# Kernel tuning notes

Hardware: AMD Instinct MI355X
Metric: run time of the kernel (lower is better)

## Reference

```python
import jax, jax.numpy as jnp
import numpy as np

EPS = 1e-6
NUM_HEADS = 16


def layer_norm(x, a, b):
    # Faithful to the custom LayerNorm: unbiased std (ddof=1), eps added to sigma.
    mu = jnp.mean(x, axis=-1, keepdims=True)
    sigma = jnp.std(x, axis=-1, keepdims=True, ddof=1) + EPS
    return (x - mu) / sigma * a + b


def entmax15(x):
    # Exact 1.5-entmax along the last axis (Peters et al. 2019, sort-based).
    S = x.shape[-1]
    x = x / 2.0
    x = x - jnp.max(x, axis=-1, keepdims=True)  # shift-invariant stabilization
    xs = jnp.flip(jnp.sort(x, axis=-1), axis=-1)  # descending
    k = jnp.arange(1, S + 1, dtype=x.dtype)
    mean = jnp.cumsum(xs, axis=-1) / k
    meansq = jnp.cumsum(xs * xs, axis=-1) / k
    ss = k * (meansq - mean * mean)
    delta = (1.0 - ss) / k
    tau = mean - jnp.sqrt(jnp.clip(delta, 0.0))
    support_size = jnp.sum((tau <= xs).astype(jnp.int32), axis=-1, keepdims=True)
    tau_star = jnp.take_along_axis(tau, support_size - 1, axis=-1)
    return jnp.clip(x - tau_star, 0.0) ** 2


def linear(x, w, b):
    return jnp.einsum('bsd,od->bso', x, w) + b


def setup_inputs() -> dict:
    key = jax.random.key(0)
    B, S, D, DFF = 1, 2048, 1024, 4096
    ks = jax.random.split(key, 12)
    p = lambda k, shape: jax.random.normal(k, shape, dtype=jnp.float32) * 0.02
    return {
        'inputs': jax.random.normal(ks[0], (B, S, D), dtype=jnp.float32),
        'mask': jax.random.randint(ks[1], (B, S), 0, 2, dtype=jnp.int32),
        'wq': p(ks[2], (D, D)), 'bq': jnp.zeros((D,), jnp.float32),
        'wk': p(ks[3], (D, D)), 'bk': jnp.zeros((D,), jnp.float32),
        'wv': p(ks[4], (D, D)), 'bv': jnp.zeros((D,), jnp.float32),
        'wo': p(ks[5], (D, D)), 'bo': jnp.zeros((D,), jnp.float32),
        'ln1_a': jnp.ones((D,), jnp.float32), 'ln1_b': jnp.zeros((D,), jnp.float32),
        'w1': p(ks[6], (DFF, D)), 'b1': jnp.zeros((DFF,), jnp.float32),
        'w2': p(ks[7], (D, DFF)), 'b2': jnp.zeros((D,), jnp.float32),
        'ln2_a': jnp.ones((D,), jnp.float32), 'ln2_b': jnp.zeros((D,), jnp.float32),
    }


def reference(inputs, mask, wq, bq, wk, bk, wv, bv, wo, bo, ln1_a, ln1_b,
              w1, b1, w2, b2, ln2_a, ln2_b):
    B, S, D = inputs.shape
    H = NUM_HEADS
    hd = D // H

    # --- Sublayer 1: pre-norm -> SparseMHA -> residual (dropout=0 -> identity) ---
    x1 = layer_norm(inputs, ln1_a, ln1_b)
    split = lambda t: t.reshape(B, S, H, hd).transpose(0, 2, 1, 3)  # [B,H,S,hd]
    q = split(linear(x1, wq, bq))
    k = split(linear(x1, wk, bk))
    v = split(linear(x1, wv, bv))

    scores = jnp.einsum('bhqd,bhkd->bhqk', q, k) / jnp.sqrt(jnp.asarray(hd, jnp.float32))
    # torch: mask.unsqueeze(0) -> (1,B,S); with B==1 it broadcasts as a key mask (1,1,1,S)
    mask4 = mask[None, None]  # (1,1,B,S), B==1
    scores = jnp.where(mask4 == 0, jnp.float32(-1e9), scores)

    p_attn = entmax15(scores).astype(jnp.float32)
    attended = jnp.einsum('bhqk,bhkd->bhqd', p_attn, v)
    attended = attended.transpose(0, 2, 1, 3).reshape(B, S, D)
    y = inputs + linear(attended, wo, bo)

    # --- Sublayer 2: pre-norm -> FFN -> residual ---
    x2 = layer_norm(y, ln2_a, ln2_b)
    ffn = linear(jax.nn.relu(linear(x2, w1, b1)), w2, b2)
    return y + ffn
```

## Files before the change

kernel.cpp:

```cpp
#include <hip/hip_runtime.h>
#include <hip/hip_bf16.h>

#define S   2048
#define D   1024
#define DFF 4096
#define NH  16
#define HD  64

typedef unsigned short u16;
typedef unsigned int   u32;
typedef __attribute__((ext_vector_type(8))) short      short8;
typedef __attribute__((ext_vector_type(4))) float      floatx4;
typedef __attribute__((ext_vector_type(2))) _Float16   half2v;
typedef __attribute__((ext_vector_type(4))) _Float16   half4v;
typedef __attribute__((ext_vector_type(8))) _Float16   half8v;

__device__ __forceinline__ float bu2f(u16 u) {
    union { u32 i; float f; } x; x.i = ((u32)u) << 16; return x.f;
}
__device__ __forceinline__ u16 f2bu(float f) {
    __hip_bfloat16 h = __float2bfloat16(f);
    return *(u16*)&h;
}
__device__ __forceinline__ u16 f2h(float f) {
    _Float16 h = (_Float16)f; return *(u16*)&h;
}
__device__ __forceinline__ float ldf(const float* p) { return *p; }
__device__ __forceinline__ float ldf(const u16* p)   { return bu2f(*p); }

__device__ __forceinline__ half2v pkrtz(float a, float b) {
    auto v = __builtin_amdgcn_cvt_pkrtz(a, b);
    union { decltype(v) i; half2v o; } u; u.i = v; return u.o;
}

__device__ __forceinline__ floatx4 mfma_f16(half8v a, half8v b, floatx4 c) {
    return __builtin_amdgcn_mfma_f32_16x16x32_f16(a, b, c, 0, 0, 0);
}
__device__ __forceinline__ float fdot2f(half2v a, half2v b, float c) {
#if __has_builtin(__builtin_amdgcn_fdot2)
    return __builtin_amdgcn_fdot2(a, b, c, false);
#else
    return c + (float)a[0] * (float)b[0] + (float)a[1] * (float)b[1];
#endif
}

template <int K>
__device__ __forceinline__ float ror16f(float v) {
    int s = __builtin_bit_cast(int, v);
    int r = __builtin_amdgcn_update_dpp(s, s, 0x120 | K, 0xF, 0xF, false);
    return __builtin_bit_cast(float, r);
}
__device__ __forceinline__ float rowsum16(float v) {
    v += ror16f<1>(v);
    v += ror16f<2>(v);
    v += ror16f<4>(v);
    v += ror16f<8>(v);
    return v;
}
__device__ __forceinline__ float rowmax16(float v) {
    v = fmaxf(v, ror16f<1>(v));
    v = fmaxf(v, ror16f<2>(v));
    v = fmaxf(v, ror16f<4>(v));
    v = fmaxf(v, ror16f<8>(v));
    return v;
}

__device__ __forceinline__ void async16(const void* g, void* l) {
    __builtin_amdgcn_global_load_lds(
        (const __attribute__((address_space(1))) u32*)g,
        (__attribute__((address_space(3))) u32*)l, 16, 0, 0);
}

__global__ __launch_bounds__(256)
void cvt_kernel(const float* __restrict__ in, u16* __restrict__ out, int n4)
{
    int i = blockIdx.x * 256 + threadIdx.x;
    if (i < n4) {
        float4 v = ((const float4*)in)[i];
        ushort4 s;
        s.x = f2bu(v.x); s.y = f2bu(v.y); s.z = f2bu(v.z); s.w = f2bu(v.w);
        ((ushort4*)out)[i] = s;
    }
}

__global__ __launch_bounds__(256)
void scan_mask_kernel(const int* __restrict__ mask, int* __restrict__ newpos,
                      int* __restrict__ nkbuf)
{
    __shared__ int ps[256];
    const int t = threadIdx.x;
    int loc[8];
    int s = 0;
#pragma unroll
    for (int j = 0; j < 8; j++) {
        loc[j] = s;
        s += (mask[t * 8 + j] != 0);
    }
    ps[t] = s;
    __syncthreads();
    for (int off = 1; off < 256; off <<= 1) {
        int v = (t >= off) ? ps[t - off] : 0;
        __syncthreads();
        ps[t] += v;
        __syncthreads();
    }
    const int total = ps[255];
    const int base = t ? ps[t - 1] : 0;
#pragma unroll
    for (int j = 0; j < 8; j++) {
        const int gi = t * 8 + j;
        const int up = base + loc[j];
        newpos[gi] = mask[gi] ? up : (total + gi - up);
    }
    if (t == 0) nkbuf[0] = total;
}

template <typename T>
__global__ __launch_bounds__(256, 4)
void ln_kernel(const T* __restrict__ in, const float* __restrict__ ga,
               const float* __restrict__ gb, u16* __restrict__ out)
{
    const int row = blockIdx.x;
    const int t = threadIdx.x;
    const T* x = in + (size_t)row * D;
    float v[4];
    float s = 0.f, ss = 0.f;
#pragma unroll
    for (int j = 0; j < 4; j++) {
        float val = ldf(x + t + 256 * j);
        v[j] = val; s += val; ss = fmaf(val, val, ss);
    }
#pragma unroll
    for (int off = 32; off >= 1; off >>= 1) {
        s  += __shfl_down(s,  off, 64);
        ss += __shfl_down(ss, off, 64);
    }
    __shared__ float red[10];
    const int wave = t >> 6, lane = t & 63;
    if (lane == 0) { red[wave] = s; red[4 + wave] = ss; }
    __syncthreads();
    if (t == 0) {
        float S1 = red[0] + red[1] + red[2] + red[3];
        float S2 = red[4] + red[5] + red[6] + red[7];
        float mu = S1 / (float)D;
        float var = (S2 - (float)D * mu * mu) / (float)(D - 1);
        float sig = sqrtf(fmaxf(var, 0.f)) + 1e-6f;
        red[8] = mu; red[9] = 1.f / sig;
    }
    __syncthreads();
    const float mu = red[8], rs = red[9];
#pragma unroll
    for (int j = 0; j < 4; j++) {
        int c = t + 256 * j;
        out[(size_t)row * D + c] = f2bu((v[j] - mu) * rs * ga[c] + gb[c]);
    }
}

#define GEMM_CORE(A_, B_, K_)                                                   \
    __shared__ u16 As[128 * 32];                                                \
    __shared__ u16 Bs[128 * 32];                                                \
    const int t = threadIdx.x;                                                  \
    const int w = t >> 6, l = t & 63;                                           \
    const int m0 = blockIdx.y * 128, n0 = blockIdx.x * 128;                     \
    const int qk = l >> 4, col = l & 15;                                        \
    const int wm = (w & 1) * 64, wn = (w >> 1) * 64;                            \
    const int sr  = l >> 2;                                                     \
    const int sq  = l & 3;                                                      \
    const int row = w * 16 + sr;                                                \
    const int gq  = sq ^ ((row >> 1) & 3);                                      \
    const u16* Ap = A_ + (size_t)(m0 + row) * K_ + gq * 8;                      \
    const u16* Bp = B_ + (size_t)(n0 + row) * K_ + gq * 8;                      \
    u16* AsW = As + w * 16 * 32;                                                \
    u16* BsW = Bs + w * 16 * 32;                                                \
    const int mloc = wm + col, nloc = wn + col;                                 \
    const u16* aBase = As + mloc * 32 + (qk ^ ((mloc >> 1) & 3)) * 8;           \
    const u16* bBase = Bs + nloc * 32 + (qk ^ ((nloc >> 1) & 3)) * 8;           \
    floatx4 acc[4][4];                                                          \
    _Pragma("unroll")                                                           \
    for (int i = 0; i < 4; i++)                                                 \
        _Pragma("unroll")                                                       \
        for (int j = 0; j < 4; j++) acc[i][j] = (floatx4)0.f;                   \
    for (int k0 = 0; k0 < K_; k0 += 32) {                                       \
        __syncthreads();                                                        \
        async16(Ap,                  AsW);                                      \
        async16(Ap + (size_t)64 * K_, AsW + 64 * 32);                           \
        async16(Bp,                  BsW);                                      \
        async16(Bp + (size_t)64 * K_, BsW + 64 * 32);                           \
        Ap += 32; Bp += 32;                                                     \
        __syncthreads();                                                        \
        short8 a[4], b[4];                                                      \
        _Pragma("unroll")                                                       \
        for (int i = 0; i < 4; i++) a[i] = *(const short8*)(aBase + i * 16 * 32);\
        _Pragma("unroll")                                                       \
        for (int j = 0; j < 4; j++) b[j] = *(const short8*)(bBase + j * 16 * 32);\
        _Pragma("unroll")                                                       \
        for (int i = 0; i < 4; i++)                                             \
            _Pragma("unroll")                                                   \
            for (int j = 0; j < 4; j++)                                         \
                acc[i][j] = __builtin_amdgcn_mfma_f32_16x16x32_bf16(            \
                    a[i], b[j], acc[i][j], 0, 0, 0);                            \
    }

template <int OMODE, bool RELU, int RES>
__global__ __launch_bounds__(256, 2)
void gemm_mfma(const u16* __restrict__ A, const u16* __restrict__ B,
               const float* __restrict__ bias, const void* __restrict__ res,
               void* __restrict__ Cout, int M, int N, int K)
{
    GEMM_CORE(A, B, K)
#pragma unroll
    for (int j = 0; j < 4; j++) {
        const int n = n0 + wn + j * 16 + col;
        const float bn = bias[n];
#pragma unroll
        for (int i = 0; i < 4; i++) {
#pragma unroll
            for (int r = 0; r < 4; r++) {
                const int m = m0 + wm + i * 16 + qk * 4 + r;
                float v = acc[i][j][r] + bn;
                if (RELU) v = fmaxf(v, 0.f);
                if (RES == 1) v += ((const float*)res)[(size_t)m * N + n];
                if (RES == 2) v += bu2f(((const u16*)res)[(size_t)m * N + n]);
                if (OMODE == 0) ((float*)Cout)[(size_t)m * N + n] = v;
                if (OMODE == 1) ((u16*)Cout)[(size_t)m * N + n] = f2bu(v);
            }
        }
    }
}

__global__ __launch_bounds__(256, 2)
void gemm_qkv(const u16* __restrict__ A, const u16* __restrict__ B,
              const float* __restrict__ bq, const float* __restrict__ bk,
              const float* __restrict__ bv, const int* __restrict__ np,
              u16* __restrict__ outQ, u16* __restrict__ outK,
              u16* __restrict__ outVT)
{
    const int K = D;
    GEMM_CORE(A, B, K)
    const int seg   = n0 >> 10;
    const int nbase = n0 & 1023;
    const float* bs = (seg == 0) ? bq : (seg == 1) ? bk : bv;
    int npm[4][4];
    if (seg != 0) {
#pragma unroll
        for (int i = 0; i < 4; i++)
#pragma unroll
            for (int r = 0; r < 4; r++)
                npm[i][r] = np[m0 + wm + i * 16 + qk * 4 + r];
    }
#pragma unroll
    for (int j = 0; j < 4; j++) {
        const int nl = nbase + wn + j * 16 + col;
        const float bn = bs[nl];
#pragma unroll
        for (int i = 0; i < 4; i++) {
#pragma unroll
            for (int r = 0; r < 4; r++) {
                const int m = m0 + wm + i * 16 + qk * 4 + r;
                float v = acc[i][j][r] + bn;
                if (seg == 0)      outQ [(size_t)m * D + nl]          = f2h(v);
                else if (seg == 1) outK [(size_t)npm[i][r] * D + nl]  = f2h(v);
                else               outVT[(size_t)nl * S + npm[i][r]]  = f2h(v);
            }
        }
    }
}

template <int OMODE, int RES>
__global__ __launch_bounds__(256, 2)
void gemm_mfma64(const u16* __restrict__ A, const u16* __restrict__ B,
                 const float* __restrict__ bias, const void* __restrict__ res,
                 void* __restrict__ Cout, int M, int N, int K)
{
    __shared__ u16 As[128 * 32];
    __shared__ u16 Bs[64 * 32];
    const int t = threadIdx.x;
    const int w = t >> 6, l = t & 63;
    const int m0 = blockIdx.y * 128, n0 = blockIdx.x * 64;
    const int qk = l >> 4, col = l & 15;
    const int wm = (w & 1) * 64, wn = (w >> 1) * 32;
    const int sr = l >> 2, sq = l & 3;
    const int row = w * 16 + sr;
    const int gq = sq ^ ((row >> 1) & 3);
    const u16* Ap = A + (size_t)(m0 + row) * K + gq * 8;
    const u16* Bp = B + (size_t)(n0 + row) * K + gq * 8;
    u16* AsW = As + w * 16 * 32;
    u16* BsW = Bs + w * 16 * 32;
    const int mloc = wm + col, nloc = wn + col;
    const u16* aBase = As + mloc * 32 + (qk ^ ((mloc >> 1) & 3)) * 8;
    const u16* bBase = Bs + nloc * 32 + (qk ^ ((nloc >> 1) & 3)) * 8;
    floatx4 acc[4][2];
#pragma unroll
    for (int i = 0; i < 4; i++)
#pragma unroll
        for (int j = 0; j < 2; j++) acc[i][j] = (floatx4)0.f;
    for (int k0 = 0; k0 < K; k0 += 32) {
        __syncthreads();
        async16(Ap, AsW);
        async16(Ap + (size_t)64 * K, AsW + 64 * 32);
        async16(Bp, BsW);
        Ap += 32; Bp += 32;
        __syncthreads();
        short8 a[4], b[2];
#pragma unroll
        for (int i = 0; i < 4; i++) a[i] = *(const short8*)(aBase + i * 16 * 32);
#pragma unroll
        for (int j = 0; j < 2; j++) b[j] = *(const short8*)(bBase + j * 16 * 32);
#pragma unroll
        for (int i = 0; i < 4; i++)
#pragma unroll
            for (int j = 0; j < 2; j++)
                acc[i][j] = __builtin_amdgcn_mfma_f32_16x16x32_bf16(
                    a[i], b[j], acc[i][j], 0, 0, 0);
    }
#pragma unroll
    for (int j = 0; j < 2; j++) {
        const int n = n0 + wn + j * 16 + col;
        const float bn = bias[n];
#pragma unroll
        for (int i = 0; i < 4; i++) {
#pragma unroll
            for (int r = 0; r < 4; r++) {
                const int m = m0 + wm + i * 16 + qk * 4 + r;
                float v = acc[i][j][r] + bn;
                if (RES == 1) v += ((const float*)res)[(size_t)m * N + n];
                if (RES == 2) v += bu2f(((const u16*)res)[(size_t)m * N + n]);
                if (OMODE == 0) ((float*)Cout)[(size_t)m * N + n] = v;
                if (OMODE == 1) ((u16*)Cout)[(size_t)m * N + n] = f2bu(v);
            }
        }
    }
}

__global__ __launch_bounds__(256, 5)
void attn_small(const u16* __restrict__ qb, const u16* __restrict__ kb,
                const u16* __restrict__ vT, const int* __restrict__ nkbuf,
                u16* __restrict__ att)
{
    const int nk = nkbuf[0];
    if (nk > 1152) return;
    __shared__ u16 Plds[16 * 1024];
    const int NS = (nk + 127) >> 7;
    const int NT = (nk + 31) >> 5;
    const int hh = blockIdx.x >> 7;
    const int q0 = (blockIdx.x & 127) * 16;
    const int t  = threadIdx.x;
    const int w  = __builtin_amdgcn_readfirstlane(t >> 6);
    const int l  = t & 63;
    const int lg = l >> 4, lc = l & 15;
    const _Float16 NEG = (_Float16)(-30000.f);
    const half4v NEG4 = {NEG, NEG, NEG, NEG};

    const u16* qp = qb + (size_t)(q0 + lc) * D + hh * HD + lg * 8;
    const half8v bq0 = *(const half8v*)qp;
    const half8v bq1 = *(const half8v*)(qp + 32);
    const u16* kbase = kb + hh * HD + lg * 8;

#pragma unroll
    for (int T = 0; T < 16; T++) {
        const int g = 4 * T + w;
        if (g < 8 * NS) {
            half4v scv;
            if ((g + 1) * 16 <= nk) {
                const u16* kp = kbase + (size_t)(g * 16 + lc) * D;
                floatx4 a = (floatx4)0.f;
                a = mfma_f16(*(const half8v*)kp,        bq0, a);
                a = mfma_f16(*(const half8v*)(kp + 32), bq1, a);
                half2v p01 = pkrtz(a[0] * 0.0625f, a[1] * 0.0625f);
                half2v p23 = pkrtz(a[2] * 0.0625f, a[3] * 0.0625f);
                scv = __builtin_shufflevector(p01, p23, 0, 1, 2, 3);
            } else if (g * 16 < nk) {
                const u16* kp = kbase + (size_t)(g * 16 + lc) * D;
                floatx4 a = (floatx4)0.f;
                a = mfma_f16(*(const half8v*)kp,        bq0, a);
                a = mfma_f16(*(const half8v*)(kp + 32), bq1, a);
                const int kb0 = g * 16 + lg * 4;
                half2v p01 = pkrtz(kb0 + 0 < nk ? a[0] * 0.0625f : -30000.f,
                                   kb0 + 1 < nk ? a[1] * 0.0625f : -30000.f);
                half2v p23 = pkrtz(kb0 + 2 < nk ? a[2] * 0.0625f : -30000.f,
                                   kb0 + 3 < nk ? a[3] * 0.0625f : -30000.f);
                scv = __builtin_shufflevector(p01, p23, 0, 1, 2, 3);
            } else {
                scv = NEG4;
            }
            const int kl = g * 16 + lg * 4;
            const int b  = kl >> 3;
            const int p  = b ^ ((b >> 3) & 7) ^ (lc & 7);
            *(half4v*)&Plds[lc * 1024 + p * 8 + (lg & 1) * 4] = scv;
        }
    }
    __syncthreads();

    const int R = 4 * w + lg;
    half8v xq[9];
#pragma unroll
    for (int s = 0; s < 8; s++) {
        if (s < NS) {
            const int b = 16 * s + lc;
            const int p = b ^ ((b >> 3) & 7) ^ (R & 7);
            xq[s] = *(const half8v*)&Plds[R * 1024 + p * 8];
        }
    }
    if (NS > 8) {
        __syncthreads();
#pragma unroll
        for (int T = 16; T < 18; T++) {
            const int g = 4 * T + w;
            half4v scv;
            if ((g + 1) * 16 <= nk) {
                const u16* kp = kbase + (size_t)(g * 16 + lc) * D;
                floatx4 a = (floatx4)0.f;
                a = mfma_f16(*(const half8v*)kp,        bq0, a);
                a = mfma_f16(*(const half8v*)(kp + 32), bq1, a);
                half2v p01 = pkrtz(a[0] * 0.0625f, a[1] * 0.0625f);
                half2v p23 = pkrtz(a[2] * 0.0625f, a[3] * 0.0625f);
                scv = __builtin_shufflevector(p01, p23, 0, 1, 2, 3);
            } else if (g * 16 < nk) {
                const u16* kp = kbase + (size_t)(g * 16 + lc) * D;
                floatx4 a = (floatx4)0.f;
                a = mfma_f16(*(const half8v*)kp,        bq0, a);
                a = mfma_f16(*(const half8v*)(kp + 32), bq1, a);
                const int kb0 = g * 16 + lg * 4;
                half2v p01 = pkrtz(kb0 + 0 < nk ? a[0] * 0.0625f : -30000.f,
                                   kb0 + 1 < nk ? a[1] * 0.0625f : -30000.f);
                half2v p23 = pkrtz(kb0 + 2 < nk ? a[2] * 0.0625f : -30000.f,
                                   kb0 + 3 < nk ? a[3] * 0.0625f : -30000.f);
                scv = __builtin_shufflevector(p01, p23, 0, 1, 2, 3);
            } else {
                scv = NEG4;
            }
            const int kl = g * 16 + lg * 4 - 1024;
            const int b  = kl >> 3;
            const int p  = b ^ ((b >> 3) & 7) ^ (lc & 7);
            *(half4v*)&Plds[lc * 1024 + p * 8 + (lg & 1) * 4] = scv;
        }
        __syncthreads();
        {
            const int b = lc;
            const int p = b ^ ((b >> 3) & 7) ^ (R & 7);
            xq[8] = *(const half8v*)&Plds[R * 1024 + p * 8];
        }
    }

    float tau;
    {
        half8v m8 = xq[0];
#pragma unroll
        for (int i = 1; i < 9; i++)
            if (i < NS) m8 = __builtin_elementwise_max(m8, xq[i]);
        union { half8v v; half2v h[4]; } u; u.v = m8;
        half2v m2 = __builtin_elementwise_max(
            __builtin_elementwise_max(u.h[0], u.h[1]),
            __builtin_elementwise_max(u.h[2], u.h[3]));
        float mx = fmaxf((float)m2[0], (float)m2[1]);
        mx = rowmax16(mx);
        tau = mx - 1.0f;
    }

    const half2v one2 = {(_Float16)1.f, (_Float16)1.f};
    const float nact = (float)(8 * NS);
#pragma unroll 1
    for (int it = 0; it < 12; it++) {
        const _Float16 th = (_Float16)tau;
        const float tf = (float)th;
        const half8v t8 = {th, th, th, th, th, th, th, th};
        float m1a = 0.f, m1b = 0.f, m2a = 0.f, m2b = 0.f;
#pragma unroll
        for (int i = 0; i < 9; i++) {
            if (i < NS) {
                union { half8v v; half2v h[4]; } u;
                u.v = __builtin_elementwise_max(xq[i], t8);
                m1a = fdot2f(u.h[0], one2, m1a);
                m2a = fdot2f(u.h[0], u.h[0], m2a);
                m1b = fdot2f(u.h[1], one2, m1b);
                m2b = fdot2f(u.h[1], u.h[1], m2b);
                m1a = fdot2f(u.h[2], one2, m1a);
                m2a = fdot2f(u.h[2], u.h[2], m2a);
                m1b = fdot2f(u.h[3], one2, m1b);
                m2b = fdot2f(u.h[3], u.h[3], m2b);
            }
        }
        const float M1 = m1a + m1b, M2 = m2a + m2b;
        float s1 = fmaf(-nact, tf, M1);
        float s2 = fmaf(tf, fmaf(nact, tf, -2.f * M1), M2);
        s1 = rowsum16(s1);
        s2 = rowsum16(s2);
        const float delta = (s2 - 1.0f) / (2.0f * fmaxf(s1, 1e-4f));
        tau += delta;
        if (__all(fabsf(delta) < 2.5e-4f)) break;
    }

    const _Float16 th = (_Float16)tau;
    const half8v t8 = {th, th, th, th, th, th, th, th};
    const half8v z8 = (half8v)(_Float16)0.f;
    floatx4 oa0 = (floatx4)0.f, oa1 = (floatx4)0.f;
    floatx4 oa2 = (floatx4)0.f, oa3 = (floatx4)0.f;
    const u16* vp = vT + (size_t)(hh * HD + w * 16 + lc) * S + lg * 8;
#pragma unroll
    for (int s = 0; s < 8; s++) {
        if (s < NS) {
            half8v dp = __builtin_elementwise_max(xq[s] - t8, z8);
            const int b = 16 * s + lc;
            const int p = b ^ ((b >> 3) & 7) ^ (R & 7);
            *(half8v*)&Plds[R * 1024 + p * 8] = dp * dp;
        }
    }
    __syncthreads();
    __builtin_amdgcn_s_setprio(1);
#pragma unroll
    for (int kt = 0; kt < 32; kt++) {
        if (kt < NT) {
            const int b = kt * 4 + lg;
            const int p = b ^ ((b >> 3) & 7) ^ (lc & 7);
            half8v af = *(const half8v*)&Plds[lc * 1024 + p * 8];
            half8v bf = *(const half8v*)(vp + kt * 32);
            if ((kt & 3) == 0)      oa0 = mfma_f16(af, bf, oa0);
            else if ((kt & 3) == 1) oa1 = mfma_f16(af, bf, oa1);
            else if ((kt & 3) == 2) oa2 = mfma_f16(af, bf, oa2);
            else                    oa3 = mfma_f16(af, bf, oa3);
        }
    }
    __builtin_amdgcn_s_setprio(0);
    if (NS > 8) {
        __syncthreads();
        {
            half8v dp = __builtin_elementwise_max(xq[8] - t8, z8);
            const int b = lc;
            const int p = b ^ ((b >> 3) & 7) ^ (R & 7);
            *(half8v*)&Plds[R * 1024 + p * 8] = dp * dp;
        }
        __syncthreads();
        const u16* vph = vp + 1024;
#pragma unroll
        for (int kt2 = 0; kt2 < 4; kt2++) {
            if (32 + kt2 < NT) {
                const int b = kt2 * 4 + lg;
                const int p = b ^ ((b >> 3) & 7) ^ (lc & 7);
                half8v af = *(const half8v*)&Plds[lc * 1024 + p * 8];
                half8v bf = *(const half8v*)(vph + kt2 * 32);
                if ((kt2 & 3) == 0)      oa0 = mfma_f16(af, bf, oa0);
                else if ((kt2 & 3) == 1) oa1 = mfma_f16(af, bf, oa1);
                else if ((kt2 & 3) == 2) oa2 = mfma_f16(af, bf, oa2);
                else                     oa3 = mfma_f16(af, bf, oa3);
            }
        }
    }
    const floatx4 oacc = (oa0 + oa1) + (oa2 + oa3);
#pragma unroll
    for (int r = 0; r < 4; r++)
        att[(size_t)(q0 + lg * 4 + r) * D + hh * HD + w * 16 + lc] = f2bu(oacc[r]);
}

__global__ __launch_bounds__(256, 5)
void attn_f16(const u16* __restrict__ qb, const u16* __restrict__ kb,
              const u16* __restrict__ vT, const int* __restrict__ nkbuf,
              u16* __restrict__ att)
{
    const int nk = nkbuf[0];
    if (nk <= 1152) return;
    __shared__ u16 Plds[16 * 1024];
    const int NS = (nk + 127) >> 7;
    const int NT = (nk + 31) >> 5;
    const int hh = blockIdx.x >> 7;
    const int q0 = (blockIdx.x & 127) * 16;
    const int t  = threadIdx.x;
    const int w  = __builtin_amdgcn_readfirstlane(t >> 6);
    const int l  = t & 63;
    const int lg = l >> 4, lc = l & 15;
    const _Float16 NEG = (_Float16)(-30000.f);

    const u16* qp = qb + (size_t)(q0 + lc) * D + hh * HD + lg * 8;
    const half8v bq0 = *(const half8v*)qp;
    const half8v bq1 = *(const half8v*)(qp + 32);

    half4v sc[32];
    {
        const u16* kbase = kb + hh * HD + lg * 8;
        __builtin_amdgcn_s_setprio(1);
#pragma unroll
        for (int T = 0; T < 32; T++) {
            const int g = 4 * T + w;
            if (g * 16 < nk) {
                const u16* kp = kbase + (size_t)(g * 16 + lc) * D;
                floatx4 a = (floatx4)0.f;
                a = mfma_f16(*(const half8v*)kp,        bq0, a);
                a = mfma_f16(*(const half8v*)(kp + 32), bq1, a);
                const int kb0 = g * 16 + lg * 4;
                half2v p01 = pkrtz(kb0 + 0 < nk ? a[0] * 0.0625f : -30000.f,
                                   kb0 + 1 < nk ? a[1] * 0.0625f : -30000.f);
                half2v p23 = pkrtz(kb0 + 2 < nk ? a[2] * 0.0625f : -30000.f,
                                   kb0 + 3 < nk ? a[3] * 0.0625f : -30000.f);
                sc[T] = __builtin_shufflevector(p01, p23, 0, 1, 2, 3);
            } else {
                sc[T] = (half4v){NEG, NEG, NEG, NEG};
            }
        }
        __builtin_amdgcn_s_setprio(0);
    }

    const int R = 4 * w + lg;
    half8v xq[16];
    {
#pragma unroll
        for (int T = 0; T < 16; T++) {
            const int g  = 4 * T + w;
            const int kl = g * 16 + lg * 4;
            const int b  = kl >> 3;
            const int p  = b ^ ((b >> 3) & 7) ^ (lc & 7);
            *(half4v*)&Plds[lc * 1024 + p * 8 + (lg & 1) * 4] = sc[T];
        }
        __syncthreads();
#pragma unroll
        for (int s = 0; s < 8; s++) {
            if (s < NS) {
                const int b = 16 * s + lc;
                const int p = b ^ ((b >> 3) & 7) ^ (R & 7);
                xq[s] = *(const half8v*)&Plds[R * 1024 + p * 8];
            }
        }
        __syncthreads();
#pragma unroll
        for (int T = 16; T < 32; T++) {
            const int g  = 4 * T + w;
            const int kl = g * 16 + lg * 4 - 1024;
            const int b  = kl >> 3;
            const int p  = b ^ ((b >> 3) & 7) ^ (lc & 7);
            *(half4v*)&Plds[lc * 1024 + p * 8 + (lg & 1) * 4] = sc[T];
        }
        __syncthreads();
#pragma unroll
        for (int s = 0; s < 8; s++) {
            const int j = 8 + s;
            if (j < NS) {
                const int b = 16 * s + lc;
                const int p = b ^ ((b >> 3) & 7) ^ (R & 7);
                xq[j] = *(const half8v*)&Plds[R * 1024 + p * 8];
            }
        }
    }

    float tau;
    {
        half8v m8 = xq[0];
#pragma unroll
        for (int i = 1; i < 16; i++)
            if (i < NS) m8 = __builtin_elementwise_max(m8, xq[i]);
        union { half8v v; half2v h[4]; } u; u.v = m8;
        half2v m2 = __builtin_elementwise_max(
            __builtin_elementwise_max(u.h[0], u.h[1]),
            __builtin_elementwise_max(u.h[2], u.h[3]));
        float mx = fmaxf((float)m2[0], (float)m2[1]);
        mx = rowmax16(mx);
        tau = mx - 1.0f;
    }

    const half2v one2 = {(_Float16)1.f, (_Float16)1.f};
    const float nact = (float)(8 * NS);
#pragma unroll 1
    for (int it = 0; it < 12; it++) {
        const _Float16 th = (_Float16)tau;
        const float tf = (float)th;
        const half8v t8 = {th, th, th, th, th, th, th, th};
        float m1a = 0.f, m1b = 0.f, m2a = 0.f, m2b = 0.f;
#pragma unroll
        for (int i = 0; i < 16; i++) {
            if (i < NS) {
                union { half8v v; half2v h[4]; } u;
                u.v = __builtin_elementwise_max(xq[i], t8);
                m1a = fdot2f(u.h[0], one2, m1a);
                m2a = fdot2f(u.h[0], u.h[0], m2a);
                m1b = fdot2f(u.h[1], one2, m1b);
                m2b = fdot2f(u.h[1], u.h[1], m2b);
                m1a = fdot2f(u.h[2], one2, m1a);
                m2a = fdot2f(u.h[2], u.h[2], m2a);
                m1b = fdot2f(u.h[3], one2, m1b);
                m2b = fdot2f(u.h[3], u.h[3], m2b);
            }
        }
        const float M1 = m1a + m1b, M2 = m2a + m2b;
        float s1 = fmaf(-nact, tf, M1);
        float s2 = fmaf(tf, fmaf(nact, tf, -2.f * M1), M2);
        s1 = rowsum16(s1);
        s2 = rowsum16(s2);
        const float delta = (s2 - 1.0f) / (2.0f * fmaxf(s1, 1e-4f));
        tau += delta;
        if (__all(fabsf(delta) < 2.5e-4f)) break;
    }

    const _Float16 th = (_Float16)tau;
    const half8v t8 = {th, th, th, th, th, th, th, th};
    const half8v z8 = (half8v)(_Float16)0.f;
    floatx4 oa0 = (floatx4)0.f, oa1 = (floatx4)0.f;
    floatx4 oa2 = (floatx4)0.f, oa3 = (floatx4)0.f;
    const u16* vp = vT + (size_t)(hh * HD + w * 16 + lc) * S + lg * 8;
#pragma unroll
    for (int s = 0; s < 8; s++) {
        if (s < NS) {
            half8v dp = __builtin_elementwise_max(xq[s] - t8, z8);
            const int b = 16 * s + lc;
            const int p = b ^ ((b >> 3) & 7) ^ (R & 7);
            *(half8v*)&Plds[R * 1024 + p * 8] = dp * dp;
        }
    }
    __syncthreads();
    __builtin_amdgcn_s_setprio(1);
#pragma unroll
    for (int kt = 0; kt < 32; kt++) {
        if (kt < NT) {
            const int b = kt * 4 + lg;
            const int p = b ^ ((b >> 3) & 7) ^ (lc & 7);
            half8v af = *(const half8v*)&Plds[lc * 1024 + p * 8];
            half8v bf = *(const half8v*)(vp + kt * 32);
            if ((kt & 3) == 0)      oa0 = mfma_f16(af, bf, oa0);
            else if ((kt & 3) == 1) oa1 = mfma_f16(af, bf, oa1);
            else if ((kt & 3) == 2) oa2 = mfma_f16(af, bf, oa2);
            else                    oa3 = mfma_f16(af, bf, oa3);
        }
    }
    __builtin_amdgcn_s_setprio(0);
    {
        __syncthreads();
#pragma unroll
        for (int s = 0; s < 8; s++) {
            const int j = 8 + s;
            if (j < NS) {
                half8v dp = __builtin_elementwise_max(xq[j] - t8, z8);
                const int b = 16 * s + lc;
                const int p = b ^ ((b >> 3) & 7) ^ (R & 7);
                *(half8v*)&Plds[R * 1024 + p * 8] = dp * dp;
            }
        }
        __syncthreads();
        const u16* vph = vp + 1024;
        __builtin_amdgcn_s_setprio(1);
#pragma unroll
        for (int kt = 0; kt < 32; kt++) {
            if (32 + kt < NT) {
                const int b = kt * 4 + lg;
                const int p = b ^ ((b >> 3) & 7) ^ (lc & 7);
                half8v af = *(const half8v*)&Plds[lc * 1024 + p * 8];
                half8v bf = *(const half8v*)(vph + kt * 32);
                if ((kt & 3) == 0)      oa0 = mfma_f16(af, bf, oa0);
                else if ((kt & 3) == 1) oa1 = mfma_f16(af, bf, oa1);
                else if ((kt & 3) == 2) oa2 = mfma_f16(af, bf, oa2);
                else                    oa3 = mfma_f16(af, bf, oa3);
            }
        }
        __builtin_amdgcn_s_setprio(0);
    }
    const floatx4 oacc = (oa0 + oa1) + (oa2 + oa3);
#pragma unroll
    for (int r = 0; r < 4; r++)
        att[(size_t)(q0 + lg * 4 + r) * D + hh * HD + w * 16 + lc] = f2bu(oacc[r]);
}

extern "C" void kernel_launch(void* const* d_in, const int* in_sizes, int n_in,
                              void* d_out, int out_size, void* d_ws, size_t ws_size,
                              hipStream_t stream)
{
    const float* inp  = (const float*)d_in[0];
    const int*   mask = (const int*)d_in[1];
    const float* wq   = (const float*)d_in[2];
    const float* bq   = (const float*)d_in[3];
    const float* wk   = (const float*)d_in[4];
    const float* bk   = (const float*)d_in[5];
    const float* wv   = (const float*)d_in[6];
    const float* bv   = (const float*)d_in[7];
    const float* wo   = (const float*)d_in[8];
    const float* bo   = (const float*)d_in[9];
    const float* ln1a = (const float*)d_in[10];
    const float* ln1b = (const float*)d_in[11];
    const float* w1   = (const float*)d_in[12];
    const float* b1   = (const float*)d_in[13];
    const float* w2   = (const float*)d_in[14];
    const float* b2   = (const float*)d_in[15];
    const float* ln2a = (const float*)d_in[16];
    const float* ln2b = (const float*)d_in[17];

    const size_t MB = 1u << 20;
    char* w = (char*)d_ws;
    u16* wqkvb = (u16*)(w + 0 * MB);
    u16* w1b   = (u16*)(w + 0 * MB);
    u16* w2b   = (u16*)(w + 0 * MB);
    u16* x1    = (u16*)(w + 8 * MB);
    u16* att   = x1;
    u16* x2    = x1;
    u16* qb_   = (u16*)(w + 12 * MB);
    u16* yb    = (u16*)(w + 12 * MB);
    u16* kb_   = (u16*)(w + 16 * MB);
    u16* vTb   = (u16*)(w + 20 * MB);
    u16* wob   = (u16*)(w + 24 * MB);
    u16* hb    = (u16*)(w + 16 * MB);
    int* np    = (int*)(w + 26 * MB);
    int* nkbuf = np + 2048;
    float* outF = (float*)d_out;

    scan_mask_kernel<<<1, 256, 0, stream>>>(mask, np, nkbuf);
    cvt_kernel<<<1024, 256, 0, stream>>>(wq, wqkvb,                   (D * D) / 4);
    cvt_kernel<<<1024, 256, 0, stream>>>(wk, wqkvb + 1024 * 1024,     (D * D) / 4);
    cvt_kernel<<<1024, 256, 0, stream>>>(wv, wqkvb + 2 * 1024 * 1024, (D * D) / 4);
    cvt_kernel<<<1024, 256, 0, stream>>>(wo, wob, (D * D) / 4);
    ln_kernel<float><<<S, 256, 0, stream>>>(inp, ln1a, ln1b, x1);
    gemm_qkv<<<dim3(3 * D / 128, S / 128), 256, 0, stream>>>(
        x1, wqkvb, bq, bk, bv, np, qb_, kb_, vTb);
    cvt_kernel<<<4096, 256, 0, stream>>>(w1, w1b, (DFF * D) / 4);
    attn_small<<<NH * (S / 16), 256, 0, stream>>>(qb_, kb_, vTb, nkbuf, att);
    attn_f16<<<NH * (S / 16), 256, 0, stream>>>(qb_, kb_, vTb, nkbuf, att);
    gemm_mfma64<1, 1><<<dim3(D / 64, S / 128), 256, 0, stream>>>(
        att, wob, bo, inp, yb, S, D, D);
    ln_kernel<u16><<<S, 256, 0, stream>>>(yb, ln2a, ln2b, x2);
    gemm_mfma<1, true, 0><<<dim3(DFF / 128, S / 128), 256, 0, stream>>>(
        x2, w1b, b1, nullptr, hb, S, DFF, D);
    cvt_kernel<<<4096, 256, 0, stream>>>(w2, w2b, (DFF * D) / 4);
    gemm_mfma64<0, 2><<<dim3(D / 64, S / 128), 256, 0, stream>>>(
        hb, w2b, b2, yb, outF, S, D, DFF);
}
```

Before: 359.7 us.

## Triple-buffer GEMM shared-memory tiles with async prefetch and vmcnt-based waits

Replaces the single-buffered load-sync-compute loop in both GEMM kernels with a 3-stage ring of LDS tiles. Global-to-LDS async loads for future K-steps are issued ahead, and readiness is tracked with explicit s_waitcnt vmcnt counts and raw barriers instead of two __syncthreads per step. This lets memory latency overlap with MFMA work. In exchange LDS use per block triples, which may limit occupancy, and correctness now relies on hand-counted wait values and on K being at least 3 tiles.

```diff
diff --git a/kernel.cpp b/kernel.cpp
--- a/kernel.cpp
+++ b/kernel.cpp
@@ -70,6 +70,11 @@
         (const __attribute__((address_space(1))) u32*)g,
         (__attribute__((address_space(3))) u32*)l, 16, 0, 0);
 }
+
+#define WAITV(N) asm volatile("s_waitcnt vmcnt(" N ")" ::: "memory")
+#define WAITL()  asm volatile("s_waitcnt lgkmcnt(0)" ::: "memory")
+#define SBAR()   __builtin_amdgcn_s_barrier()
+#define SCHED0() __builtin_amdgcn_sched_barrier(0)
 
 __global__ __launch_bounds__(256)
 void cvt_kernel(const float* __restrict__ in, u16* __restrict__ out, int n4)
@@ -157,8 +162,8 @@
 }
 
 #define GEMM_CORE(A_, B_, K_)                                                   \
-    __shared__ u16 As[128 * 32];                                                \
-    __shared__ u16 Bs[128 * 32];                                                \
+    __shared__ u16 As[3 * 128 * 32];                                            \
+    __shared__ u16 Bs[3 * 128 * 32];                                            \
     const int t = threadIdx.x;                                                  \
     const int w = t >> 6, l = t & 63;                                           \
     const int m0 = blockIdx.y * 128, n0 = blockIdx.x * 128;                     \
@@ -173,32 +178,65 @@
     u16* AsW = As + w * 16 * 32;                                                \
     u16* BsW = Bs + w * 16 * 32;                                                \
     const int mloc = wm + col, nloc = wn + col;                                 \
-    const u16* aBase = As + mloc * 32 + (qk ^ ((mloc >> 1) & 3)) * 8;           \
-    const u16* bBase = Bs + nloc * 32 + (qk ^ ((nloc >> 1) & 3)) * 8;           \
+    const int aoff = mloc * 32 + (qk ^ ((mloc >> 1) & 3)) * 8;                  \
+    const int boff = nloc * 32 + (qk ^ ((nloc >> 1) & 3)) * 8;                  \
     floatx4 acc[4][4];                                                          \
     _Pragma("unroll")                                                           \
     for (int i = 0; i < 4; i++)                                                 \
         _Pragma("unroll")                                                       \
         for (int j = 0; j < 4; j++) acc[i][j] = (floatx4)0.f;                   \
-    for (int k0 = 0; k0 < K_; k0 += 32) {                                       \
-        __syncthreads();                                                        \
-        async16(Ap,                  AsW);                                      \
-        async16(Ap + (size_t)64 * K_, AsW + 64 * 32);                           \
-        async16(Bp,                  BsW);                                      \
-        async16(Bp + (size_t)64 * K_, BsW + 64 * 32);                           \
+    const int NT_ = K_ / 32;                                                    \
+    _Pragma("unroll")                                                           \
+    for (int s = 0; s < 3; s++) {                                               \
+        async16(Ap,                   AsW + s * 4096);                          \
+        async16(Ap + (size_t)64 * K_, AsW + s * 4096 + 64 * 32);                \
+        async16(Bp,                   BsW + s * 4096);                          \
+        async16(Bp + (size_t)64 * K_, BsW + s * 4096 + 64 * 32);                \
         Ap += 32; Bp += 32;                                                     \
-        __syncthreads();                                                        \
+    }                                                                           \
+    WAITV("8"); SCHED0(); SBAR();                                               \
+    int cur = 0;                                                                \
+    for (int t0 = 0; t0 + 3 < NT_; ++t0) {                                      \
         short8 a[4], b[4];                                                      \
+        const u16* aB = As + cur * 4096 + aoff;                                 \
+        const u16* bB = Bs + cur * 4096 + boff;                                 \
         _Pragma("unroll")                                                       \
-        for (int i = 0; i < 4; i++) a[i] = *(const short8*)(aBase + i * 16 * 32);\
+        for (int i = 0; i < 4; i++) a[i] = *(const short8*)(aB + i * 16 * 32);  \
         _Pragma("unroll")                                                       \
-        for (int j = 0; j < 4; j++) b[j] = *(const short8*)(bBase + j * 16 * 32);\
+        for (int j = 0; j < 4; j++) b[j] = *(const short8*)(bB + j * 16 * 32);  \
+        WAITL(); SCHED0(); SBAR();                                              \
+        async16(Ap,                   AsW + cur * 4096);                        \
+        async16(Ap + (size_t)64 * K_, AsW + cur * 4096 + 64 * 32);              \
+        async16(Bp,                   BsW + cur * 4096);                        \
+        async16(Bp + (size_t)64 * K_, BsW + cur * 4096 + 64 * 32);              \
+        Ap += 32; Bp += 32;                                                     \
         _Pragma("unroll")                                                       \
         for (int i = 0; i < 4; i++)                                             \
             _Pragma("unroll")                                                   \
             for (int j = 0; j < 4; j++)                                         \
                 acc[i][j] = __builtin_amdgcn_mfma_f32_16x16x32_bf16(            \
                     a[i], b[j], acc[i][j], 0, 0, 0);                            \
+        WAITV("8"); SCHED0(); SBAR();                                           \
+        cur = cur + 1; if (cur == 3) cur = 0;                                   \
+    }                                                                           \
+    _Pragma("unroll")                                                           \
+    for (int tail = 0; tail < 3; tail++) {                                      \
+        short8 a[4], b[4];                                                      \
+        const u16* aB = As + cur * 4096 + aoff;                                 \
+        const u16* bB = Bs + cur * 4096 + boff;                                 \
+        _Pragma("unroll")                                                       \
+        for (int i = 0; i < 4; i++) a[i] = *(const short8*)(aB + i * 16 * 32);  \
+        _Pragma("unroll")                                                       \
+        for (int j = 0; j < 4; j++) b[j] = *(const short8*)(bB + j * 16 * 32);  \
+        _Pragma("unroll")                                                       \
+        for (int i = 0; i < 4; i++)                                             \
+            _Pragma("unroll")                                                   \
+            for (int j = 0; j < 4; j++)                                         \
+                acc[i][j] = __builtin_amdgcn_mfma_f32_16x16x32_bf16(            \
+                    a[i], b[j], acc[i][j], 0, 0, 0);                            \
+        if (tail == 0) { WAITV("4"); SCHED0(); SBAR(); }                        \
+        if (tail == 1) { WAITV("0"); SCHED0(); SBAR(); }                        \
+        cur = cur + 1; if (cur == 3) cur = 0;                                   \
     }
 
 template <int OMODE, bool RELU, int RES>
@@ -272,8 +310,8 @@
                  const float* __restrict__ bias, const void* __restrict__ res,
                  void* __restrict__ Cout, int M, int N, int K)
 {
-    __shared__ u16 As[128 * 32];
-    __shared__ u16 Bs[64 * 32];
+    __shared__ u16 As[3 * 128 * 32];
+    __shared__ u16 Bs[3 * 64 * 32];
     const int t = threadIdx.x;
     const int w = t >> 6, l = t & 63;
     const int m0 = blockIdx.y * 128, n0 = blockIdx.x * 64;
@@ -287,31 +325,63 @@
     u16* AsW = As + w * 16 * 32;
     u16* BsW = Bs + w * 16 * 32;
     const int mloc = wm + col, nloc = wn + col;
-    const u16* aBase = As + mloc * 32 + (qk ^ ((mloc >> 1) & 3)) * 8;
-    const u16* bBase = Bs + nloc * 32 + (qk ^ ((nloc >> 1) & 3)) * 8;
+    const int aoff = mloc * 32 + (qk ^ ((mloc >> 1) & 3)) * 8;
+    const int boff = nloc * 32 + (qk ^ ((nloc >> 1) & 3)) * 8;
     floatx4 acc[4][2];
 #pragma unroll
     for (int i = 0; i < 4; i++)
 #pragma unroll
         for (int j = 0; j < 2; j++) acc[i][j] = (floatx4)0.f;
-    for (int k0 = 0; k0 < K; k0 += 32) {
-        __syncthreads();
-        async16(Ap, AsW);
-        async16(Ap + (size_t)64 * K, AsW + 64 * 32);
-        async16(Bp, BsW);
+    const int NT_ = K / 32;
+#pragma unroll
+    for (int s = 0; s < 3; s++) {
+        async16(Ap,                  AsW + s * 4096);
+        async16(Ap + (size_t)64 * K, AsW + s * 4096 + 64 * 32);
+        async16(Bp,                  BsW + s * 2048);
         Ap += 32; Bp += 32;
-        __syncthreads();
+    }
+    WAITV("6"); SCHED0(); SBAR();
+    int cur = 0;
+    for (int t0 = 0; t0 + 3 < NT_; ++t0) {
         short8 a[4], b[2];
-#pragma unroll
-        for (int i = 0; i < 4; i++) a[i] = *(const short8*)(aBase + i * 16 * 32);
-#pragma unroll
-        for (int j = 0; j < 2; j++) b[j] = *(const short8*)(bBase + j * 16 * 32);
+        const u16* aB = As + cur * 4096 + aoff;
+        const u16* bB = Bs + cur * 2048 + boff;
+#pragma unroll
+        for (int i = 0; i < 4; i++) a[i] = *(const short8*)(aB + i * 16 * 32);
+#pragma unroll
+        for (int j = 0; j < 2; j++) b[j] = *(const short8*)(bB + j * 16 * 32);
+        WAITL(); SCHED0(); SBAR();
+        async16(Ap,                  AsW + cur * 4096);
+        async16(Ap + (size_t)64 * K, AsW + cur * 4096 + 64 * 32);
+        async16(Bp,                  BsW + cur * 2048);
+        Ap += 32; Bp += 32;
 #pragma unroll
         for (int i = 0; i < 4; i++)
 #pragma unroll
             for (int j = 0; j < 2; j++)
                 acc[i][j] = __builtin_amdgcn_mfma_f32_16x16x32_bf16(
                     a[i], b[j], acc[i][j], 0, 0, 0);
+        WAITV("6"); SCHED0(); SBAR();
+        cur = cur + 1; if (cur == 3) cur = 0;
+    }
+#pragma unroll
+    for (int tail = 0; tail < 3; tail++) {
+        short8 a[4], b[2];
+        const u16* aB = As + cur * 4096 + aoff;
+        const u16* bB = Bs + cur * 2048 + boff;
+#pragma unroll
+        for (int i = 0; i < 4; i++) a[i] = *(const short8*)(aB + i * 16 * 32);
+#pragma unroll
+        for (int j = 0; j < 2; j++) b[j] = *(const short8*)(bB + j * 16 * 32);
+#pragma unroll
+        for (int i = 0; i < 4; i++)
+#pragma unroll
+            for (int j = 0; j < 2; j++)
+                acc[i][j] = __builtin_amdgcn_mfma_f32_16x16x32_bf16(
+                    a[i], b[j], acc[i][j], 0, 0, 0);
+        if (tail == 0) { WAITV("3"); SCHED0(); SBAR(); }
+        if (tail == 1) { WAITV("0"); SCHED0(); SBAR(); }
+        cur = cur + 1; if (cur == 3) cur = 0;
     }
 #pragma unroll
     for (int j = 0; j < 2; j++) {
```

After: 340.5 us. 5.3% less time.
